# Kernel tuning notes

Measured on AMD Instinct MI355X. Metric: run time of the kernel, lower is better.

## Reference

```python
import jax, jax.numpy as jnp
import numpy as np
import math

B, S, D, H, DFF = 4, 1024, 1024, 16, 4096
DK = D // H
EPS = 1e-6


def setup_inputs() -> dict:
    key = jax.random.key(0)
    ks = jax.random.split(key, 8)
    sc = 1.0 / math.sqrt(D)
    return {
        "x": jax.random.normal(ks[0], (B, S, D), jnp.float32),
        "src_mask": jnp.ones((B, 1, 1, S), jnp.int32),
        "wq": jax.random.normal(ks[1], (D, D), jnp.float32) * sc,
        "bq": jnp.zeros((D,), jnp.float32),
        "wk": jax.random.normal(ks[2], (D, D), jnp.float32) * sc,
        "bk": jnp.zeros((D,), jnp.float32),
        "wv": jax.random.normal(ks[3], (D, D), jnp.float32) * sc,
        "bv": jnp.zeros((D,), jnp.float32),
        "wo": jax.random.normal(ks[4], (D, D), jnp.float32) * sc,
        "bo": jnp.zeros((D,), jnp.float32),
        "w1": jax.random.normal(ks[5], (D, DFF), jnp.float32) * sc,
        "b1": jnp.zeros((DFF,), jnp.float32),
        "w2": jax.random.normal(ks[6], (DFF, D), jnp.float32) * (1.0 / math.sqrt(DFF)),
        "b2": jnp.zeros((D,), jnp.float32),
        "alpha1": jnp.ones((1,), jnp.float32),
        "beta1": jnp.zeros((1,), jnp.float32),
        "alpha2": jnp.ones((1,), jnp.float32),
        "beta2": jnp.zeros((1,), jnp.float32),
    }


def layer_norm(x, alpha, beta):
    # Faithful to the custom LayerNormalization: scalar alpha/beta,
    # torch std (unbiased, ddof=1), eps added to std (not variance).
    mean = jnp.mean(x, axis=-1, keepdims=True)
    std = jnp.std(x, axis=-1, keepdims=True, ddof=1)
    return alpha * (x - mean) / (std + EPS) + beta


def encoder_block(x, src_mask, wq, bq, wk, bk, wv, bv, wo, bo,
                  w1, b1, w2, b2, alpha1, beta1, alpha2, beta2):
    # --- residual 1: pre-norm self-attention (dropout = 0 / eval mode) ---
    xn = layer_norm(x, alpha1, beta1)
    q = (xn @ wq + bq).reshape(B, S, H, DK).transpose(0, 2, 1, 3)  # bhsd
    k = (xn @ wk + bk).reshape(B, S, H, DK).transpose(0, 2, 1, 3)
    v = (xn @ wv + bv).reshape(B, S, H, DK).transpose(0, 2, 1, 3)
    scores = jnp.einsum("bhqd,bhkd->bhqk", q, k) / math.sqrt(DK)
    scores = jnp.where(src_mask == 0, jnp.float32(-1e9), scores)
    attn = jax.nn.softmax(scores, axis=-1)
    ctx = jnp.einsum("bhqk,bhkd->bhqd", attn, v)
    ctx = ctx.transpose(0, 2, 1, 3).reshape(B, S, D)
    x = x + (ctx @ wo + bo)
    # --- residual 2: pre-norm feed-forward ---
    xn2 = layer_norm(x, alpha2, beta2)
    ff = jax.nn.relu(xn2 @ w1 + b1) @ w2 + b2
    return x + ff


def reference(x, src_mask, wq, bq, wk, bk, wv, bv, wo, bo,
              w1, b1, w2, b2, alpha1, beta1, alpha2, beta2):
    return encoder_block(x, src_mask, wq, bq, wk, bk, wv, bv, wo, bo,
                         w1, b1, w2, b2, alpha1, beta1, alpha2, beta2)
```

## Files before the change

### kernel.cpp

```cpp
#include <hip/hip_runtime.h>
#include <hip/hip_bf16.h>
#include <stdint.h>


typedef unsigned short u16;
typedef __attribute__((ext_vector_type(4))) float f32x4;
typedef __attribute__((ext_vector_type(8))) short bf16x8;
typedef __attribute__((ext_vector_type(4))) unsigned short u16x4;

__device__ __forceinline__ u16 f2b(float f) {
  unsigned int u = __builtin_bit_cast(unsigned int, f);
  u += 0x7FFFu + ((u >> 16) & 1u);
  return (u16)(u >> 16);
}

__device__ __forceinline__ void gload_lds16(const void* g, void* l) {
  __builtin_amdgcn_global_load_lds(
      reinterpret_cast<__attribute__((address_space(1))) void*>(
          reinterpret_cast<uintptr_t>(g)),
      reinterpret_cast<__attribute__((address_space(3))) void*>(
          reinterpret_cast<uintptr_t>(l)),
      16, 0, 0);
}

#define MFMA16(a, b, c) __builtin_amdgcn_mfma_f32_16x16x32_bf16((a), (b), (c), 0, 0, 0)

__global__ __launch_bounds__(256) void cast_transpose(
    const float* __restrict__ in, u16* __restrict__ out, int K, int N) {
  __shared__ float tile[32][33];
  const int n0 = blockIdx.x * 32, k0 = blockIdx.y * 32;
  const int tx = threadIdx.x & 31, ty = threadIdx.x >> 5;
#pragma unroll
  for (int i = 0; i < 32; i += 8)
    tile[ty + i][tx] = in[(int64_t)(k0 + ty + i) * N + (n0 + tx)];
  __syncthreads();
#pragma unroll
  for (int i = 0; i < 32; i += 8)
    out[(int64_t)(n0 + ty + i) * K + (k0 + tx)] = f2b(tile[tx][ty + i]);
}

__global__ void pack_bias(const float* __restrict__ bq, const float* __restrict__ bk,
                          const float* __restrict__ bv, float* __restrict__ out) {
  int i = blockIdx.x * 256 + threadIdx.x;
  const float* src = (i < 1024) ? bq : (i < 2048 ? bk : bv);
  out[i] = src[i & 1023];
}

__global__ __launch_bounds__(256) void transpose_v(
    const u16* __restrict__ qkv, u16* __restrict__ vt) {
  __shared__ u16 t[32][33];
  const int bh = blockIdx.z;
  const int b = bh >> 4, h = bh & 15;
  const int s0 = blockIdx.x * 32, d0 = blockIdx.y * 32;
  const int tx = threadIdx.x & 31, ty = threadIdx.x >> 5;
  const u16* src = qkv + (int64_t)(b * 1024) * 3072 + 2048 + h * 64;
#pragma unroll
  for (int i = 0; i < 32; i += 8)
    t[ty + i][tx] = src[(int64_t)(s0 + ty + i) * 3072 + d0 + tx];
  __syncthreads();
  u16* dst = vt + (int64_t)bh * 64 * 1024;
#pragma unroll
  for (int i = 0; i < 32; i += 8)
    dst[(int64_t)(d0 + ty + i) * 1024 + s0 + tx] = t[tx][ty + i];
}

__global__ __launch_bounds__(256) void layernorm_k(
    const float* __restrict__ x, const float* __restrict__ alpha,
    const float* __restrict__ beta, u16* __restrict__ out) {
  const int row = blockIdx.x;
  const float4 v = ((const float4*)(x + (int64_t)row * 1024))[threadIdx.x];
  float s = v.x + v.y + v.z + v.w;
  float sq = v.x * v.x + v.y * v.y + v.z * v.z + v.w * v.w;
#pragma unroll
  for (int off = 1; off < 64; off <<= 1) {
    s += __shfl_xor(s, off, 64);
    sq += __shfl_xor(sq, off, 64);
  }
  __shared__ float ss[4], ssq[4];
  const int wid = threadIdx.x >> 6;
  if ((threadIdx.x & 63) == 0) { ss[wid] = s; ssq[wid] = sq; }
  __syncthreads();
  s = ss[0] + ss[1] + ss[2] + ss[3];
  sq = ssq[0] + ssq[1] + ssq[2] + ssq[3];
  const float mean = s * (1.0f / 1024.0f);
  float var = (sq - 1024.0f * mean * mean) * (1.0f / 1023.0f);
  var = fmaxf(var, 0.0f);
  const float inv = alpha[0] / (sqrtf(var) + 1e-6f);
  const float bt = beta[0];
  u16x4 o;
  o[0] = f2b((v.x - mean) * inv + bt);
  o[1] = f2b((v.y - mean) * inv + bt);
  o[2] = f2b((v.z - mean) * inv + bt);
  o[3] = f2b((v.w - mean) * inv + bt);
  *(u16x4*)(out + (int64_t)row * 1024 + threadIdx.x * 4) = o;
}

template <int BN, bool OUT_BF16, bool RELU, bool RES, bool QSCALE = false>
__global__ __launch_bounds__(256) void gemm_bt(
    const u16* __restrict__ A, const u16* __restrict__ Bt,
    const float* __restrict__ bias, const float* __restrict__ res,
    void* __restrict__ Cout, int Ndim, int K) {
  constexpr int NF = BN / 32;
  __shared__ u16 Alds[2][128 * 32];
  __shared__ u16 Blds[2][BN * 32];
  const int tid = threadIdx.x;
  const int wid = tid >> 6, lane = tid & 63;
  int flat = blockIdx.y * gridDim.x + blockIdx.x;
  const int cpx = (gridDim.x * gridDim.y) >> 3;
  flat = (flat & 7) * cpx + (flat >> 3);
  const int bm0 = (flat / gridDim.x) * 128;
  const int bn0 = (flat % gridDim.x) * BN;
  const int wm = (wid >> 1) * 64, wn = (wid & 1) * (BN / 2);
  const int lrow = lane & 15, lg = lane >> 4;

  f32x4 acc[4][NF] = {};

  const int srow = tid >> 2, skoff = (tid & 3) * 8;
  const u16* Ag = A + (int64_t)(bm0 + srow) * K + skoff;
  const u16* Bg = Bt + (int64_t)(bn0 + srow) * K + skoff;
  const int64_t half = (int64_t)64 * K;

  auto stage = [&](int buf) {
    char* ad = (char*)&Alds[buf][0] + tid * 16;
    char* bd = (char*)&Blds[buf][0] + tid * 16;
    gload_lds16(Ag, ad);
    gload_lds16(Ag + half, ad + 4096);
    gload_lds16(Bg, bd);
    if (BN == 128) gload_lds16(Bg + half, bd + 4096);
    Ag += 32; Bg += 32;
  };

  const int nK = K >> 5;
  stage(0);
  __syncthreads();
  int cur = 0;
  for (int kt = 0; kt < nK; ++kt) {
    if (kt + 1 < nK) stage(cur ^ 1);
    bf16x8 af[4], bfr[NF];
#pragma unroll
    for (int f = 0; f < 4; ++f)
      af[f] = *(const bf16x8*)&Alds[cur][(wm + f * 16 + lrow) * 32 + lg * 8];
#pragma unroll
    for (int f = 0; f < NF; ++f)
      bfr[f] = *(const bf16x8*)&Blds[cur][(wn + f * 16 + lrow) * 32 + lg * 8];
#pragma unroll
    for (int mf = 0; mf < 4; ++mf)
#pragma unroll
      for (int nf = 0; nf < NF; ++nf)
        acc[mf][nf] = MFMA16(af[mf], bfr[nf], acc[mf][nf]);
    __syncthreads();
    cur ^= 1;
  }

#pragma unroll
  for (int mf = 0; mf < 4; ++mf) {
#pragma unroll
    for (int nf = 0; nf < NF; ++nf) {
      const int col = bn0 + wn + nf * 16 + lrow;
      const float bv = bias[col];
#pragma unroll
      for (int r = 0; r < 4; ++r) {
        const int row = bm0 + wm + mf * 16 + lg * 4 + r;
        float v = acc[mf][nf][r] + bv;
        if (QSCALE && col < 1024) v *= 0.125f;
        if (RELU) v = fmaxf(v, 0.0f);
        if (RES) v += res[(int64_t)row * Ndim + col];
        if (OUT_BF16)
          ((u16*)Cout)[(int64_t)row * Ndim + col] = f2b(v);
        else
          ((float*)Cout)[(int64_t)row * Ndim + col] = v;
      }
    }
  }
}

__global__ __launch_bounds__(256) void attention_k(
    const u16* __restrict__ qkv, const u16* __restrict__ vt,
    const int* __restrict__ mask, u16* __restrict__ ctxout) {
  int flat = blockIdx.y * gridDim.x + blockIdx.x;
  flat = (flat & 7) * 128 + (flat >> 3);
  const int bh = flat >> 4;
  const int q0 = (flat & 15) * 64;
  const int b = bh >> 4, h = bh & 15;
  const int tid = threadIdx.x, wid = tid >> 6, lane = tid & 63;
  const int lrow = lane & 15, lg = lane >> 4;

  __shared__ u16 Klds[2][64 * 64];
  __shared__ u16 Vtlds[2][64 * 64];
  __shared__ u16 Plds[4][16 * 68];

  const int64_t rs = 3072;
  const u16* Qb = qkv + (int64_t)(b * 1024) * rs + h * 64;
  const u16* Kb = Qb + 1024;
  const u16* Vtb = vt + (int64_t)bh * 64 * 1024;

  bf16x8 qf[2];
  {
    const u16* qp = Qb + (int64_t)(q0 + wid * 16 + lrow) * rs + lg * 8;
    qf[0] = *(const bf16x8*)qp;
    qf[1] = *(const bf16x8*)(qp + 32);
  }

  const int c0 = wid * 64 + lane, c1 = 256 + c0;
  const int r0 = c0 >> 3, r1 = c1 >> 3;
  const int gq0 = (c0 & 7) ^ (r0 & 7), gq1 = (c1 & 7) ^ (r1 & 7);
  const u16* Kg0 = Kb + (int64_t)r0 * rs + gq0 * 8;
  const u16* Kg1 = Kb + (int64_t)r1 * rs + gq1 * 8;
  const u16* Vg0 = Vtb + r0 * 1024 + gq0 * 8;
  const u16* Vg1 = Vtb + r1 * 1024 + gq1 * 8;

  float m[4], l[4];
  f32x4 ctx[4] = {};
#pragma unroll
  for (int r = 0; r < 4; ++r) { m[r] = -1e30f; l[r] = 0.0f; }

  auto stageKV = [&](int buf, int kt) {
    const int sk0 = kt * 64;
    char* kd = (char*)&Klds[buf][0] + wid * 1024;
    char* vd = (char*)&Vtlds[buf][0] + wid * 1024;
    gload_lds16(Kg0 + (int64_t)sk0 * rs, kd);
    gload_lds16(Kg1 + (int64_t)sk0 * rs, kd + 4096);
    gload_lds16(Vg0 + sk0, vd);
    gload_lds16(Vg1 + sk0, vd + 4096);
  };

  stageKV(0, 0);
  __syncthreads();
  int cur = 0;
  for (int kt = 0; kt < 16; ++kt) {
    if (kt + 1 < 16) stageKV(cur ^ 1, kt + 1);
    const u16* Kc = &Klds[cur][0];
    const u16* Vc = &Vtlds[cur][0];
    const int sk0 = kt * 64;

    f32x4 sa[4];
#pragma unroll
    for (int nf = 0; nf < 4; ++nf) {
      const int srow = nf * 16 + lrow;
      const char* kr = (const char*)Kc + srow * 128;
      bf16x8 kf0 = *(const bf16x8*)(kr + ((lg ^ (srow & 7)) * 16));
      bf16x8 kf1 = *(const bf16x8*)(kr + (((4 | lg) ^ (srow & 7)) * 16));
      f32x4 a = {};
      a = MFMA16(qf[0], kf0, a);
      a = MFMA16(qf[1], kf1, a);
      sa[nf] = a;
    }
#pragma unroll
    for (int nf = 0; nf < 4; ++nf) {
      const int mval = mask[b * 1024 + sk0 + nf * 16 + lrow];
#pragma unroll
      for (int r = 0; r < 4; ++r)
        sa[nf][r] = (mval == 0) ? -1e9f : sa[nf][r];
    }
    float mxs[4];
#pragma unroll
    for (int r = 0; r < 4; ++r) {
      float mx = fmaxf(fmaxf(sa[0][r], sa[1][r]), fmaxf(sa[2][r], sa[3][r]));
#pragma unroll
      for (int off = 1; off < 16; off <<= 1) mx = fmaxf(mx, __shfl_xor(mx, off, 64));
      mxs[r] = mx;
    }
    float growth = mxs[0] - m[0];
#pragma unroll
    for (int r = 1; r < 4; ++r) growth = fmaxf(growth, mxs[r] - m[r]);
    if (!__all(growth <= 8.0f)) {
#pragma unroll
      for (int r = 0; r < 4; ++r) {
        const float mn = fmaxf(m[r], mxs[r]);
        const float fac = __expf(m[r] - mn);
        m[r] = mn;
        l[r] *= fac;
#pragma unroll
        for (int df = 0; df < 4; ++df) ctx[df][r] *= fac;
      }
    }
    float rsum[4] = {0.f, 0.f, 0.f, 0.f};
    u16 pb[4][4];
#pragma unroll
    for (int nf = 0; nf < 4; ++nf)
#pragma unroll
      for (int r = 0; r < 4; ++r) {
        const float p = __expf(sa[nf][r] - m[r]);
        rsum[r] += p;
        pb[nf][r] = f2b(p);
      }
#pragma unroll
    for (int r = 0; r < 4; ++r) {
      float t = rsum[r];
#pragma unroll
      for (int off = 1; off < 16; off <<= 1) t += __shfl_xor(t, off, 64);
      l[r] += t;
    }
    u16* P = &Plds[wid][0];
#pragma unroll
    for (int nf = 0; nf < 4; ++nf)
#pragma unroll
      for (int r = 0; r < 4; ++r)
        P[(lg * 4 + r) * 68 + nf * 16 + lrow] = pb[nf][r];
    bf16x8 pf0 = *(const bf16x8*)&P[lrow * 68 + lg * 8];
    bf16x8 pf1 = *(const bf16x8*)&P[lrow * 68 + 32 + lg * 8];
#pragma unroll
    for (int df = 0; df < 4; ++df) {
      const int drow = df * 16 + lrow;
      const char* vr = (const char*)Vc + drow * 128;
      bf16x8 vf0 = *(const bf16x8*)(vr + ((lg ^ (drow & 7)) * 16));
      bf16x8 vf1 = *(const bf16x8*)(vr + (((4 | lg) ^ (drow & 7)) * 16));
      ctx[df] = MFMA16(pf0, vf0, ctx[df]);
      ctx[df] = MFMA16(pf1, vf1, ctx[df]);
    }
    __syncthreads();
    cur ^= 1;
  }
#pragma unroll
  for (int df = 0; df < 4; ++df)
#pragma unroll
    for (int r = 0; r < 4; ++r) {
      const int row = b * 1024 + q0 + wid * 16 + lg * 4 + r;
      const int col = h * 64 + df * 16 + lrow;
      ctxout[(int64_t)row * 1024 + col] = f2b(ctx[df][r] / l[r]);
    }
}

extern "C" void kernel_launch(void* const* d_in, const int* in_sizes, int n_in,
                              void* d_out, int out_size, void* d_ws, size_t ws_size,
                              hipStream_t stream) {
  (void)in_sizes; (void)n_in; (void)out_size; (void)ws_size;
  const float* x      = (const float*)d_in[0];
  const int*   mask   = (const int*)d_in[1];
  const float* wq     = (const float*)d_in[2];
  const float* bq     = (const float*)d_in[3];
  const float* wk     = (const float*)d_in[4];
  const float* bk     = (const float*)d_in[5];
  const float* wv     = (const float*)d_in[6];
  const float* bv     = (const float*)d_in[7];
  const float* wo     = (const float*)d_in[8];
  const float* bo     = (const float*)d_in[9];
  const float* w1     = (const float*)d_in[10];
  const float* b1     = (const float*)d_in[11];
  const float* w2     = (const float*)d_in[12];
  const float* b2     = (const float*)d_in[13];
  const float* alpha1 = (const float*)d_in[14];
  const float* beta1  = (const float*)d_in[15];
  const float* alpha2 = (const float*)d_in[16];
  const float* beta2  = (const float*)d_in[17];
  float* out = (float*)d_out;

  char* ws = (char*)d_ws;
  u16*   wqkvT = (u16*)ws;                 ws += (size_t)3072 * 1024 * 2;
  u16*   woT   = (u16*)ws;                 ws += (size_t)1024 * 1024 * 2;
  u16*   w1T   = (u16*)ws;                 ws += (size_t)4096 * 1024 * 2;
  u16*   w2T   = (u16*)ws;                 ws += (size_t)1024 * 4096 * 2;
  float* bqkv  = (float*)ws;               ws += 16384;
  u16*   xn    = (u16*)ws;                 ws += (size_t)4096 * 1024 * 2;
  u16*   qkv   = (u16*)ws;                 ws += (size_t)4096 * 3072 * 2;
  u16*   ctx   = (u16*)ws;                 ws += (size_t)4096 * 1024 * 2;
  float* x2    = (float*)ws;               ws += (size_t)4096 * 1024 * 4;
  u16*   vtb   = (u16*)ws;                 ws += (size_t)64 * 64 * 1024 * 2;
  u16*   hbuf  = qkv;

  const dim3 blk(256);
  cast_transpose<<<dim3(32, 32), blk, 0, stream>>>(wq, wqkvT, 1024, 1024);
  cast_transpose<<<dim3(32, 32), blk, 0, stream>>>(wk, wqkvT + 1024 * 1024, 1024, 1024);
  cast_transpose<<<dim3(32, 32), blk, 0, stream>>>(wv, wqkvT + 2048 * 1024, 1024, 1024);
  cast_transpose<<<dim3(32, 32), blk, 0, stream>>>(wo, woT, 1024, 1024);
  cast_transpose<<<dim3(128, 32), blk, 0, stream>>>(w1, w1T, 1024, 4096);
  cast_transpose<<<dim3(32, 128), blk, 0, stream>>>(w2, w2T, 4096, 1024);
  pack_bias<<<dim3(12), blk, 0, stream>>>(bq, bk, bv, bqkv);
  layernorm_k<<<4096, blk, 0, stream>>>(x, alpha1, beta1, xn);
  gemm_bt<128, true, false, false, true><<<dim3(24, 32), blk, 0, stream>>>(
      xn, wqkvT, bqkv, nullptr, qkv, 3072, 1024);
  transpose_v<<<dim3(32, 2, 64), blk, 0, stream>>>(qkv, vtb);
  attention_k<<<dim3(16, 64), blk, 0, stream>>>(qkv, vtb, mask, ctx);
  gemm_bt<64, false, false, true><<<dim3(16, 32), blk, 0, stream>>>(
      ctx, woT, bo, x, x2, 1024, 1024);
  layernorm_k<<<4096, blk, 0, stream>>>(x2, alpha2, beta2, xn);
  gemm_bt<128, true, true, false><<<dim3(32, 32), blk, 0, stream>>>(
      xn, w1T, b1, nullptr, hbuf, 4096, 1024);
  gemm_bt<64, false, false, true><<<dim3(16, 32), blk, 0, stream>>>(
      hbuf, w2T, b2, x2, out, 1024, 4096);
}
```

Before: 392.8 us.

## Load K and V fragments directly from global memory in attention, dropping LDS staging

The attention kernel no longer stages K and V tiles into double-buffered shared memory with async global-to-LDS loads. Each wave now reads its MFMA operand fragments straight from global memory into registers, which removes the per-iteration block barrier and frees LDS. A launch-bounds hint of 4 blocks per CU is added to raise occupancy. The trade-off is that all four waves in a block fetch the same K/V data redundantly, relying on L1/L2 hits, and global-load latency is exposed with no explicit prefetch.

After: 432.5 us. +10.1%, slower.

```diff
diff --git a/kernel.cpp b/kernel.cpp
--- a/kernel.cpp
+++ b/kernel.cpp
@@ -174,7 +174,7 @@
   }
 }
 
-__global__ __launch_bounds__(256) void attention_k(
+__global__ __launch_bounds__(256, 4) void attention_k(
     const u16* __restrict__ qkv, const u16* __restrict__ vt,
     const int* __restrict__ mask, u16* __restrict__ ctxout) {
   int flat = blockIdx.y * gridDim.x + blockIdx.x;
@@ -185,8 +185,6 @@
   const int tid = threadIdx.x, wid = tid >> 6, lane = tid & 63;
   const int lrow = lane & 15, lg = lane >> 4;
 
-  __shared__ u16 Klds[2][64 * 64];
-  __shared__ u16 Vtlds[2][64 * 64];
   __shared__ u16 Plds[4][16 * 68];
 
   const int64_t rs = 3072;
@@ -201,49 +199,37 @@
     qf[1] = *(const bf16x8*)(qp + 32);
   }
 
-  const int c0 = wid * 64 + lane, c1 = 256 + c0;
-  const int r0 = c0 >> 3, r1 = c1 >> 3;
-  const int gq0 = (c0 & 7) ^ (r0 & 7), gq1 = (c1 & 7) ^ (r1 & 7);
-  const u16* Kg0 = Kb + (int64_t)r0 * rs + gq0 * 8;
-  const u16* Kg1 = Kb + (int64_t)r1 * rs + gq1 * 8;
-  const u16* Vg0 = Vtb + r0 * 1024 + gq0 * 8;
-  const u16* Vg1 = Vtb + r1 * 1024 + gq1 * 8;
+  const u16* Kbase = Kb + (int64_t)lrow * rs + lg * 8;
+  const u16* Vbase = Vtb + lrow * 1024 + lg * 8;
 
   float m[4], l[4];
   f32x4 ctx[4] = {};
 #pragma unroll
   for (int r = 0; r < 4; ++r) { m[r] = -1e30f; l[r] = 0.0f; }
 
-  auto stageKV = [&](int buf, int kt) {
+  for (int kt = 0; kt < 16; ++kt) {
     const int sk0 = kt * 64;
-    char* kd = (char*)&Klds[buf][0] + wid * 1024;
-    char* vd = (char*)&Vtlds[buf][0] + wid * 1024;
-    gload_lds16(Kg0 + (int64_t)sk0 * rs, kd);
-    gload_lds16(Kg1 + (int64_t)sk0 * rs, kd + 4096);
-    gload_lds16(Vg0 + sk0, vd);
-    gload_lds16(Vg1 + sk0, vd + 4096);
-  };
-
-  stageKV(0, 0);
-  __syncthreads();
-  int cur = 0;
-  for (int kt = 0; kt < 16; ++kt) {
-    if (kt + 1 < 16) stageKV(cur ^ 1, kt + 1);
-    const u16* Kc = &Klds[cur][0];
-    const u16* Vc = &Vtlds[cur][0];
-    const int sk0 = kt * 64;
-
+    bf16x8 kf0[4], kf1[4];
+#pragma unroll
+    for (int nf = 0; nf < 4; ++nf) {
+      const u16* kp = Kbase + (int64_t)(sk0 + nf * 16) * rs;
+      kf0[nf] = *(const bf16x8*)kp;
+      kf1[nf] = *(const bf16x8*)(kp + 32);
+    }
     f32x4 sa[4];
 #pragma unroll
     for (int nf = 0; nf < 4; ++nf) {
-      const int srow = nf * 16 + lrow;
-      const char* kr = (const char*)Kc + srow * 128;
-      bf16x8 kf0 = *(const bf16x8*)(kr + ((lg ^ (srow & 7)) * 16));
-      bf16x8 kf1 = *(const bf16x8*)(kr + (((4 | lg) ^ (srow & 7)) * 16));
       f32x4 a = {};
-      a = MFMA16(qf[0], kf0, a);
-      a = MFMA16(qf[1], kf1, a);
+      a = MFMA16(qf[0], kf0[nf], a);
+      a = MFMA16(qf[1], kf1[nf], a);
       sa[nf] = a;
+    }
+    bf16x8 vf0[4], vf1[4];
+#pragma unroll
+    for (int df = 0; df < 4; ++df) {
+      const u16* vp = Vbase + df * 16 * 1024 + sk0;
+      vf0[df] = *(const bf16x8*)vp;
+      vf1[df] = *(const bf16x8*)(vp + 32);
     }
 #pragma unroll
     for (int nf = 0; nf < 4; ++nf) {
@@ -301,15 +287,9 @@
     bf16x8 pf1 = *(const bf16x8*)&P[lrow * 68 + 32 + lg * 8];
 #pragma unroll
     for (int df = 0; df < 4; ++df) {
-      const int drow = df * 16 + lrow;
-      const char* vr = (const char*)Vc + drow * 128;
-      bf16x8 vf0 = *(const bf16x8*)(vr + ((lg ^ (drow & 7)) * 16));
-      bf16x8 vf1 = *(const bf16x8*)(vr + (((4 | lg) ^ (drow & 7)) * 16));
-      ctx[df] = MFMA16(pf0, vf0, ctx[df]);
-      ctx[df] = MFMA16(pf1, vf1, ctx[df]);
-    }
-    __syncthreads();
-    cur ^= 1;
+      ctx[df] = MFMA16(pf0, vf0[df], ctx[df]);
+      ctx[df] = MFMA16(pf1, vf1[df], ctx[df]);
+    }
   }
 #pragma unroll
   for (int df = 0; df < 4; ++df)
```
